# Kernel tuning notes

Measured on AMD Instinct MI355X. Metric: run time of the kernel, lower is better.

The kernel has to match this reference:

```python
import jax, jax.numpy as jnp
import numpy as np

NG, NPG, NF = 256, 64, 64          # graphs, nodes/graph, features (NPG == NF: x is per-graph [N,N])
HC, NL = 504, 4                     # hidden_channels, num_layers (HC*NL == TRIU)
E_PER = 1024                        # edges per graph
ALPHA = 0.5
EPS = 1e-5
TRIU = NF * (NF - 1) // 2           # 2016 strict-upper-triangle entries
HIDDEN, NCLS = 1024, 2


def _bn(x, g, b):
    # BatchNorm1d in training mode: biased batch statistics
    m = x.mean(0)
    v = x.var(0)
    return (x - m) * jax.lax.rsqrt(v + EPS) * g + b


def _gcn(x, src, dst, W, b):
    n = x.shape[0]
    xw = x @ W
    deg = jax.ops.segment_sum(jnp.ones(src.shape[0], x.dtype), dst, num_segments=n) + 1.0
    dinv = jax.lax.rsqrt(deg)
    coef = (dinv[src] * dinv[dst])[:, None]
    agg = jax.ops.segment_sum(xw[src] * coef, dst, num_segments=n)
    return agg + xw * (dinv * dinv)[:, None] + b


def _pool(x, batch):
    # global_mean_pool; every graph has exactly NPG nodes
    return jax.ops.segment_sum(x, batch, num_segments=NG) / NPG


def setup_inputs():
    key = jax.random.key(0)
    ks = jax.random.split(key, 16)
    total = NG * NPG
    x = jax.random.normal(ks[0], (total, NF), jnp.float32)
    offs = (jnp.arange(NG) * NPG)[:, None]
    edge_src = (jax.random.randint(ks[1], (NG, E_PER), 0, NPG) + offs).reshape(-1)
    edge_dst = (jax.random.randint(ks[2], (NG, E_PER), 0, NPG) + offs).reshape(-1)
    batch = jnp.arange(total) // NPG

    def lin(k, fi, fo):
        return jax.random.normal(k, (fi, fo), jnp.float32) / np.sqrt(fi)

    Wg0 = lin(ks[3], NF, HC)
    bg0 = jnp.zeros((HC,), jnp.float32)
    Wg_rest = jax.random.normal(ks[4], (NL - 1, HC, HC), jnp.float32) / np.sqrt(HC)
    bg_rest = jnp.zeros((NL - 1, HC), jnp.float32)
    gx = jnp.ones((TRIU,), jnp.float32); bx = jnp.zeros((TRIU,), jnp.float32)
    gh = jnp.ones((HC * NL,), jnp.float32); bh = jnp.zeros((HC * NL,), jnp.float32)
    Watt = lin(ks[5], TRIU, 1); batt = jnp.zeros((1,), jnp.float32)
    D1 = TRIU + HC * NL  # 4032
    Wm1 = lin(ks[6], D1, HIDDEN); bm1 = jnp.zeros((HIDDEN,), jnp.float32)
    gm1 = jnp.ones((HIDDEN,), jnp.float32); bem1 = jnp.zeros((HIDDEN,), jnp.float32)
    Wm2 = lin(ks[7], HIDDEN, HIDDEN // 2); bm2 = jnp.zeros((HIDDEN // 2,), jnp.float32)
    gm2 = jnp.ones((HIDDEN // 2,), jnp.float32); bem2 = jnp.zeros((HIDDEN // 2,), jnp.float32)
    Wm3 = lin(ks[8], HIDDEN // 2, HIDDEN // 2); bm3 = jnp.zeros((HIDDEN // 2,), jnp.float32)
    gm3 = jnp.ones((HIDDEN // 2,), jnp.float32); bem3 = jnp.zeros((HIDDEN // 2,), jnp.float32)
    Wm4 = lin(ks[9], HIDDEN // 2, NCLS); bm4 = jnp.zeros((NCLS,), jnp.float32)
    return dict(x=x, Wg0=Wg0, bg0=bg0, Wg_rest=Wg_rest, bg_rest=bg_rest, gx=gx, bx=bx,
                gh=gh, bh=bh, Watt=Watt, batt=batt, Wm1=Wm1, bm1=bm1, gm1=gm1, bem1=bem1,
                Wm2=Wm2, bm2=bm2, gm2=gm2, bem2=bem2, Wm3=Wm3, bm3=bm3, gm3=gm3, bem3=bem3,
                Wm4=Wm4, bm4=bm4, edge_src=edge_src, edge_dst=edge_dst, batch=batch)


def reference(x, Wg0, bg0, Wg_rest, bg_rest, gx, bx, gh, bh, Watt, batt,
              Wm1, bm1, gm1, bem1, Wm2, bm2, gm2, bem2, Wm3, bm3, gm3, bem3,
              Wm4, bm4, edge_src, edge_dst, batch):
    # stacked GCN convs (no nonlinearity between convs, as in source)
    cur = _gcn(x, edge_src, edge_dst, Wg0, bg0)
    hs = [_pool(cur, batch)]
    for i in range(NL - 1):
        cur = _gcn(cur, edge_src, edge_dst, Wg_rest[i], bg_rest[i])
        hs.append(_pool(cur, batch))
    h = _bn(jnp.concatenate(hs, axis=1), gh, bh)          # [NG, HC*NL]
    # per-graph strict upper triangle of the [N,N] input matrix (== triu().nonzero() trick)
    iu, ju = jnp.triu_indices(NF, k=1)
    xv = x.reshape(NG, NPG, NF)[:, iu, ju]                # [NG, TRIU]
    xv = _bn(xv, gx, bx)
    att = jax.nn.sigmoid(xv @ Watt + batt)                # [NG, 1]
    xf = att * xv + (1.0 - att) * h * ALPHA               # attention-weighted fusion
    z = jnp.concatenate([xf, h], axis=1)                  # [NG, TRIU + HC*NL]
    z = jax.nn.relu(_bn(z @ Wm1 + bm1, gm1, bem1))
    z = jax.nn.relu(_bn(z @ Wm2 + bm2, gm2, bem2))
    z = jax.nn.relu(_bn(z @ Wm3 + bm3, gm3, bem3))
    return z @ Wm4 + bm4                                   # [NG, NCLS]
```

## Files before the change

### kernel.cpp

```cpp
#include <hip/hip_runtime.h>
#include <math.h>

#define NGRAPH 256
#define NPG 64
#define NFEAT 64
#define HC 504
#define NLAY 4
#define EPER 1024
#define NTRIU 2016
#define DCAT 4032
#define HID1 1024
#define HID2 512

#define GCN_LDS (65536 + 73728 + 18432)
#define AHL_LO 4608

typedef __attribute__((ext_vector_type(8))) short bfrag8;
typedef __attribute__((ext_vector_type(4))) float f32x4;

struct __align__(8) us4 { unsigned short a, b, c, d; };

__device__ __forceinline__ unsigned short f2b(float f) {
    union { float f; unsigned u; } v; v.f = f;
    unsigned r = (v.u + 0x7fffu + ((v.u >> 16) & 1u)) >> 16;
    return (unsigned short)r;
}
__device__ __forceinline__ float b2f(unsigned short h) {
    union { unsigned u; float f; } v; v.u = ((unsigned)h) << 16;
    return v.f;
}

__global__ void conv_gcn(const float* __restrict__ Wg0, const float* __restrict__ WgR,
                         unsigned short* __restrict__ Wt0, unsigned short* __restrict__ Wt123)
{
    const int z = blockIdx.z;
    const float* W;
    unsigned short* W4;
    int K, KL;
    if (z == 0) {
        if (blockIdx.y >= 2) return;
        W = Wg0; W4 = Wt0; K = 64; KL = 64;
    } else {
        W = WgR + (size_t)(z - 1) * HC * HC;
        W4 = Wt123 + (size_t)(z - 1) * 262144;
        K = HC; KL = 512;
    }
    __shared__ float T[32][33];
    int k0 = blockIdx.y * 32, n0 = blockIdx.x * 32;
    int tx = threadIdx.x, ty = threadIdx.y;
#pragma unroll
    for (int j = 0; j < 32; j += 8) {
        int k = k0 + ty + j, n = n0 + tx;
        T[ty + j][tx] = (k < K && n < HC) ? W[(size_t)k * HC + n] : 0.f;
    }
    __syncthreads();
#pragma unroll
    for (int j = 0; j < 32; j += 8) {
        int n = n0 + ty + j, k = k0 + tx;
        int idx = ((n >> 4) * (KL >> 5) + (k >> 5)) * 512
                + (((k >> 3) & 3) << 7) + ((n & 15) << 3) + (k & 7);
        W4[idx] = f2b(T[tx][ty + j]);
    }
}

__global__ void conv_mlp(const float* __restrict__ Wm1, const float* __restrict__ Wm2,
                         const float* __restrict__ Wm3,
                         unsigned short* __restrict__ W1t, unsigned short* __restrict__ W2t,
                         unsigned short* __restrict__ W3t)
{
    const int z = blockIdx.z;
    const float* W;
    unsigned short* Wt;
    int K, N;
    if (z == 0)      { W = Wm1; Wt = W1t; K = DCAT; N = HID1; }
    else if (z == 1) { W = Wm2; Wt = W2t; K = HID1; N = HID2; }
    else             { W = Wm3; Wt = W3t; K = HID2; N = HID2; }
    int k0 = blockIdx.y * 32, n0 = blockIdx.x * 32;
    if (k0 >= K || n0 >= N) return;
    __shared__ float T[32][33];
    int tx = threadIdx.x, ty = threadIdx.y;
#pragma unroll
    for (int j = 0; j < 32; j += 8) {
        int k = k0 + ty + j, n = n0 + tx;
        T[ty + j][tx] = (k < K && n < N) ? W[(size_t)k * N + n] : 0.f;
    }
    __syncthreads();
#pragma unroll
    for (int j = 0; j < 32; j += 8) {
        int n = n0 + ty + j, k = k0 + tx;
        Wt[(size_t)n * K + k] = f2b(T[tx][ty + j]);
    }
}

template<int KL>
__device__ __forceinline__ void gcn_layer(const unsigned short* __restrict__ W4,
                                          const float* __restrict__ bias,
                                          unsigned short* cur, unsigned short* xwt,
                                          const unsigned short* ahl,
                                          float* __restrict__ hsg,
                                          int wv, int lm, int lh)
{
    constexpr int KTS = KL >> 5;
    const int colw = wv << 5;
    const int kswz = (lm & 7) << 3;
    const int lane8 = ((lh << 4) + lm) << 3;

    f32x4 acc[4][2];
#pragma unroll
    for (int m0 = 0; m0 < 4; ++m0)
#pragma unroll
        for (int cc = 0; cc < 2; ++cc) acc[m0][cc] = (f32x4){0.f, 0.f, 0.f, 0.f};

    bfrag8 bq[2][2];
#pragma unroll
    for (int cc = 0; cc < 2; ++cc)
        bq[0][cc] = *(const bfrag8*)(const void*)&W4[(size_t)((wv * 2 + cc) * KTS + 0) * 512 + lane8];
    if (KTS > 1) {
#pragma unroll
        for (int cc = 0; cc < 2; ++cc)
            bq[1][cc] = *(const bfrag8*)(const void*)&W4[(size_t)((wv * 2 + cc) * KTS + 1) * 512 + lane8];
    }
#pragma unroll
    for (int kt = 0; kt < KTS; ++kt) {
        bfrag8 a[4];
#pragma unroll
        for (int m0 = 0; m0 < 4; ++m0)
            a[m0] = *(const bfrag8*)(const void*)&cur[(m0 * 16 + lm) * 512 + ((kt * 32 + (lh << 3)) ^ kswz)];
        bfrag8 bc[2];
        bc[0] = bq[kt & 1][0]; bc[1] = bq[kt & 1][1];
        if (kt + 2 < KTS) {
#pragma unroll
            for (int cc = 0; cc < 2; ++cc)
                bq[kt & 1][cc] = *(const bfrag8*)(const void*)&W4[(size_t)((wv * 2 + cc) * KTS + kt + 2) * 512 + lane8];
        }
#pragma unroll
        for (int cc = 0; cc < 2; ++cc)
#pragma unroll
            for (int m0 = 0; m0 < 4; ++m0)
                acc[m0][cc] = __builtin_amdgcn_mfma_f32_16x16x32_bf16(a[m0], bc[cc], acc[m0][cc], 0, 0, 0);
    }
    __syncthreads();

#pragma unroll
    for (int cc = 0; cc < 2; ++cc) {
        const int c = colw + cc * 16 + lm;
#pragma unroll
        for (int m0 = 0; m0 < 4; ++m0) {
            us4 p;
            p.a = f2b(acc[m0][cc][0]); p.b = f2b(acc[m0][cc][1]);
            p.c = f2b(acc[m0][cc][2]); p.d = f2b(acc[m0][cc][3]);
            *(us4*)(void*)&xwt[c * 72 + m0 * 16 + (lh << 2)] = p;
        }
    }

    f32x4 acc2[2][4];
#pragma unroll
    for (int cc = 0; cc < 2; ++cc)
#pragma unroll
        for (int n0 = 0; n0 < 4; ++n0) acc2[cc][n0] = (f32x4){0.f, 0.f, 0.f, 0.f};
#pragma unroll
    for (int n0 = 0; n0 < 4; ++n0) {
        const int o = (n0 * 16 + lm) * 72 + (lh << 3);
        bfrag8 bh0 = *(const bfrag8*)(const void*)&ahl[o];
        bfrag8 bh1 = *(const bfrag8*)(const void*)&ahl[o + 32];
        bfrag8 bl0 = *(const bfrag8*)(const void*)&ahl[AHL_LO + o];
        bfrag8 bl1 = *(const bfrag8*)(const void*)&ahl[AHL_LO + o + 32];
#pragma unroll
        for (int cc = 0; cc < 2; ++cc) {
            const int c = colw + cc * 16 + lm;
            bfrag8 a0 = *(const bfrag8*)(const void*)&xwt[c * 72 + (lh << 3)];
            bfrag8 a1 = *(const bfrag8*)(const void*)&xwt[c * 72 + 32 + (lh << 3)];
            acc2[cc][n0] = __builtin_amdgcn_mfma_f32_16x16x32_bf16(a0, bh0, acc2[cc][n0], 0, 0, 0);
            acc2[cc][n0] = __builtin_amdgcn_mfma_f32_16x16x32_bf16(a0, bl0, acc2[cc][n0], 0, 0, 0);
            acc2[cc][n0] = __builtin_amdgcn_mfma_f32_16x16x32_bf16(a1, bh1, acc2[cc][n0], 0, 0, 0);
            acc2[cc][n0] = __builtin_amdgcn_mfma_f32_16x16x32_bf16(a1, bl1, acc2[cc][n0], 0, 0, 0);
        }
    }

#pragma unroll
    for (int cc = 0; cc < 2; ++cc) {
        const int cb = colw + cc * 16 + (lh << 2);
        float bv[4];
#pragma unroll
        for (int r = 0; r < 4; ++r) {
            int c = cb + r;
            bv[r] = (c < HC) ? bias[c] : 0.f;
        }
        float t0 = 0.f, t1 = 0.f, t2 = 0.f, t3 = 0.f;
#pragma unroll
        for (int n0 = 0; n0 < 4; ++n0) {
            const int d = n0 * 16 + lm;
            float v0 = acc2[cc][n0][0] + bv[0];
            float v1 = acc2[cc][n0][1] + bv[1];
            float v2 = acc2[cc][n0][2] + bv[2];
            float v3 = acc2[cc][n0][3] + bv[3];
            t0 += v0; t1 += v1; t2 += v2; t3 += v3;
            us4 p;
            p.a = f2b(v0); p.b = f2b(v1); p.c = f2b(v2); p.d = f2b(v3);
            *(us4*)(void*)&cur[d * 512 + (cb ^ ((d & 7) << 3))] = p;
        }
#pragma unroll
        for (int m = 1; m < 16; m <<= 1) {
            t0 += __shfl_xor(t0, m, 64);
            t1 += __shfl_xor(t1, m, 64);
            t2 += __shfl_xor(t2, m, 64);
            t3 += __shfl_xor(t3, m, 64);
        }
        if (lm == 0 && cb < HC)
            *(float4*)&hsg[cb] = make_float4(t0 * (1.0f / 64.0f), t1 * (1.0f / 64.0f),
                                             t2 * (1.0f / 64.0f), t3 * (1.0f / 64.0f));
    }
    __syncthreads();
}

__global__ __launch_bounds__(1024, 4) void gcn_all(const float* __restrict__ x,
                                                   const int* __restrict__ esrc,
                                                   const int* __restrict__ edst,
                                                   const unsigned short* __restrict__ Wt0,
                                                   const unsigned short* __restrict__ Wt123,
                                                   const float* __restrict__ bg0,
                                                   const float* __restrict__ bgR,
                                                   float* __restrict__ hs)
{
    extern __shared__ char lds[];
    unsigned short* cur = (unsigned short*)lds;
    unsigned short* xwt = (unsigned short*)(lds + 65536);
    unsigned short* ahl = (unsigned short*)(lds + 65536 + 73728);
    float* Af   = (float*)(lds + 65536);
    int*   cnt  = (int*)(lds + 65536 + 16384);
    float* dinv = (float*)(lds + 65536 + 16384 + 256);

    const int g = blockIdx.x, tid = threadIdx.x;
    const int wv = tid >> 6, lane = tid & 63;
    const int lm = lane & 15, lh = lane >> 4;

    for (int i = tid; i < 4096; i += 1024) Af[i] = 0.f;
    if (tid < 64) cnt[tid] = 0;
    __syncthreads();
    atomicAdd(&cnt[edst[(size_t)g * EPER + tid] & 63], 1);
    __syncthreads();
    if (tid < 64) dinv[tid] = rsqrtf((float)cnt[tid] + 1.0f);
    __syncthreads();
    {
        int s = esrc[(size_t)g * EPER + tid] & 63;
        int d = edst[(size_t)g * EPER + tid] & 63;
        atomicAdd(&Af[d * 64 + s], dinv[s] * dinv[d]);
    }
    __syncthreads();
    if (tid < 64) Af[tid * 64 + tid] += dinv[tid] * dinv[tid];
    __syncthreads();
    for (int i = tid; i < 4096; i += 1024) {
        float v = Af[i];
        unsigned short h = f2b(v);
        int d = i >> 6, s = i & 63;
        ahl[d * 72 + s] = h;
        ahl[AHL_LO + d * 72 + s] = f2b(v - b2f(h));
    }
    {
        float4 v = ((const float4*)(x + (size_t)g * 4096))[tid];
        int row = (tid * 4) >> 6, col = (tid * 4) & 63;
        unsigned short* p = &cur[row * 512 + (col ^ ((row & 7) << 3))];
        p[0] = f2b(v.x); p[1] = f2b(v.y); p[2] = f2b(v.z); p[3] = f2b(v.w);
    }
    __syncthreads();

    float* hsg = hs + (size_t)g * (HC * NLAY);
    gcn_layer<64>(Wt0, bg0, cur, xwt, ahl, hsg, wv, lm, lh);
    for (int l = 1; l < NLAY; ++l)
        gcn_layer<512>(Wt123 + (size_t)(l - 1) * 262144, bgR + (l - 1) * HC,
                       cur, xwt, ahl, hsg + l * HC, wv, lm, lh);
}

__global__ __launch_bounds__(256) void pre_stats(const float* __restrict__ hs,
                                                 const float* __restrict__ x,
                                                 float* __restrict__ xv,
                                                 float* __restrict__ psh,
                                                 float* __restrict__ pssh,
                                                 float* __restrict__ psx,
                                                 float* __restrict__ pssx)
{
    int t = blockIdx.x * 256 + threadIdx.x;
    if (t >= NTRIU) return;
    int g0 = blockIdx.y * 16;
    if (blockIdx.z == 0) {
        float s = 0.f, ss = 0.f;
        for (int g = g0; g < g0 + 16; ++g) {
            float v = hs[(size_t)g * NTRIU + t];
            s += v; ss += v * v;
        }
        psh [(size_t)blockIdx.y * NTRIU + t] = s;
        pssh[(size_t)blockIdx.y * NTRIU + t] = ss;
    } else {
        int i = (int)(63.5f - sqrtf(63.5f * 63.5f - 2.0f * (float)t));
        while (63 * (i + 1) - (i + 1) * i / 2 <= t) ++i;
        while (63 * i - i * (i - 1) / 2 > t) --i;
        int j = t - (63 * i - i * (i - 1) / 2) + i + 1;
        int o = i * 64 + j;
        float s = 0.f, ss = 0.f;
        for (int g = g0; g < g0 + 16; ++g) {
            float v = x[(size_t)g * 4096 + o];
            xv[(size_t)g * NTRIU + t] = v;
            s += v; ss += v * v;
        }
        psx [(size_t)blockIdx.y * NTRIU + t] = s;
        pssx[(size_t)blockIdx.y * NTRIU + t] = ss;
    }
}

__global__ __launch_bounds__(256) void stats_fin2(const float* __restrict__ psh,
                                                  const float* __restrict__ pssh,
                                                  const float* __restrict__ psx,
                                                  const float* __restrict__ pssx,
                                                  float* __restrict__ hm,
                                                  float* __restrict__ hiv,
                                                  float* __restrict__ xm,
                                                  float* __restrict__ xi)
{
    int f = blockIdx.x * 256 + threadIdx.x;
    if (f >= NTRIU) return;
    const float* ps  = blockIdx.y ? psx  : psh;
    const float* pss = blockIdx.y ? pssx : pssh;
    float* mo = blockIdx.y ? xm : hm;
    float* io = blockIdx.y ? xi : hiv;
    float s = 0.f, ss = 0.f;
    for (int b = 0; b < 16; ++b) {
        s  += ps [(size_t)b * NTRIU + f];
        ss += pss[(size_t)b * NTRIU + f];
    }
    float m = s * (1.0f / NGRAPH);
    mo[f] = m;
    io[f] = rsqrtf(ss * (1.0f / NGRAPH) - m * m + 1e-5f);
}

__global__ __launch_bounds__(256) void attz_fused(const float* __restrict__ xv,
                                                  const float* __restrict__ xm,
                                                  const float* __restrict__ xi,
                                                  const float* __restrict__ gx,
                                                  const float* __restrict__ bx,
                                                  const float* __restrict__ hsrc,
                                                  const float* __restrict__ hm,
                                                  const float* __restrict__ hi,
                                                  const float* __restrict__ gh,
                                                  const float* __restrict__ bh,
                                                  const float* __restrict__ Watt,
                                                  const float* __restrict__ batt,
                                                  unsigned short* __restrict__ zhi,
                                                  unsigned short* __restrict__ zlo)
{
    int g = blockIdx.x;
    __shared__ float xs[NTRIU];
    __shared__ float red[256];
    float s = 0.f;
    for (int t = threadIdx.x; t < NTRIU; t += 256) {
        float v = (xv[(size_t)g * NTRIU + t] - xm[t]) * xi[t] * gx[t] + bx[t];
        xs[t] = v;
        s += v * Watt[t];
    }
    red[threadIdx.x] = s;
    __syncthreads();
    for (int w = 128; w > 0; w >>= 1) {
        if (threadIdx.x < w) red[threadIdx.x] += red[threadIdx.x + w];
        __syncthreads();
    }
    float att = 1.0f / (1.0f + expf(-(red[0] + batt[0])));
    for (int t = threadIdx.x; t < NTRIU; t += 256) {
        float hn = (hsrc[(size_t)g * NTRIU + t] - hm[t]) * hi[t] * gh[t] + bh[t];
        float zf = att * xs[t] + (1.0f - att) * hn * 0.5f;
        unsigned short h0 = f2b(zf);
        zhi[(size_t)g * DCAT + t] = h0;
        zlo[(size_t)g * DCAT + t] = f2b(zf - b2f(h0));
        unsigned short h1 = f2b(hn);
        zhi[(size_t)g * DCAT + NTRIU + t] = h1;
        zlo[(size_t)g * DCAT + NTRIU + t] = f2b(hn - b2f(h1));
    }
}

__global__ __launch_bounds__(256) void gemm_bf_sk(const unsigned short* __restrict__ Ahi,
                                                  const unsigned short* __restrict__ Alo,
                                                  const unsigned short* __restrict__ Bt,
                                                  float* __restrict__ P,
                                                  int N, int K, int chunk)
{
    __shared__ unsigned short Ah[2][2048], Al[2][2048], Bs[2][2048];
    const int tid  = threadIdx.x;
    const int wave = tid >> 6, lane = tid & 63;
    const int row0 = blockIdx.y << 6, col0 = blockIdx.x << 6;
    const int kb = blockIdx.z * chunk;
    const int NT = chunk >> 5;
    const int sr = tid >> 2, sk = (tid & 3) << 3;
    const unsigned short* gAh = Ahi + (size_t)(row0 + sr) * K + kb + sk;
    const unsigned short* gAl = Alo + (size_t)(row0 + sr) * K + kb + sk;
    const unsigned short* gB  = Bt  + (size_t)(col0 + sr) * K + kb + sk;

    int4 rh = *(const int4*)(const void*)gAh;
    int4 rl = *(const int4*)(const void*)gAl;
    int4 rb = *(const int4*)(const void*)gB;
    *(int4*)(void*)&Ah[0][tid << 3] = rh;
    *(int4*)(void*)&Al[0][tid << 3] = rl;
    *(int4*)(void*)&Bs[0][tid << 3] = rb;
    __syncthreads();

    f32x4 acc0 = {0.f, 0.f, 0.f, 0.f};
    f32x4 acc1 = acc0, acc2 = acc0, acc3 = acc0;
    const int aoff = (wave * 16 + (lane & 15)) * 32 + ((lane >> 4) << 3);
    const int boff = (lane & 15) * 32 + ((lane >> 4) << 3);

    for (int t = 0; t < NT; ++t) {
        if (t + 1 < NT) {
            rh = *(const int4*)(const void*)(gAh + (t + 1) * 32);
            rl = *(const int4*)(const void*)(gAl + (t + 1) * 32);
            rb = *(const int4*)(const void*)(gB  + (t + 1) * 32);
        }
        const unsigned short* ah = Ah[t & 1];
        const unsigned short* al = Al[t & 1];
        const unsigned short* bs = Bs[t & 1];
        bfrag8 a  = *(const bfrag8*)(const void*)&ah[aoff];
        bfrag8 a2 = *(const bfrag8*)(const void*)&al[aoff];
        bfrag8 b0 = *(const bfrag8*)(const void*)&bs[boff];
        bfrag8 b1 = *(const bfrag8*)(const void*)&bs[boff + 16 * 32];
        bfrag8 b2 = *(const bfrag8*)(const void*)&bs[boff + 32 * 32];
        bfrag8 b3 = *(const bfrag8*)(const void*)&bs[boff + 48 * 32];
        acc0 = __builtin_amdgcn_mfma_f32_16x16x32_bf16(a,  b0, acc0, 0, 0, 0);
        acc0 = __builtin_amdgcn_mfma_f32_16x16x32_bf16(a2, b0, acc0, 0, 0, 0);
        acc1 = __builtin_amdgcn_mfma_f32_16x16x32_bf16(a,  b1, acc1, 0, 0, 0);
        acc1 = __builtin_amdgcn_mfma_f32_16x16x32_bf16(a2, b1, acc1, 0, 0, 0);
        acc2 = __builtin_amdgcn_mfma_f32_16x16x32_bf16(a,  b2, acc2, 0, 0, 0);
        acc2 = __builtin_amdgcn_mfma_f32_16x16x32_bf16(a2, b2, acc2, 0, 0, 0);
        acc3 = __builtin_amdgcn_mfma_f32_16x16x32_bf16(a,  b3, acc3, 0, 0, 0);
        acc3 = __builtin_amdgcn_mfma_f32_16x16x32_bf16(a2, b3, acc3, 0, 0, 0);
        if (t + 1 < NT) {
            *(int4*)(void*)&Ah[(t + 1) & 1][tid << 3] = rh;
            *(int4*)(void*)&Al[(t + 1) & 1][tid << 3] = rl;
            *(int4*)(void*)&Bs[(t + 1) & 1][tid << 3] = rb;
        }
        __syncthreads();
    }

    float* Pp = P + (size_t)blockIdx.z * NGRAPH * N;
    const int rbase = row0 + wave * 16 + ((lane >> 4) << 2);
    const int cbase = col0 + (lane & 15);
#pragma unroll
    for (int r = 0; r < 4; ++r) {
        int grow = rbase + r;
        Pp[(size_t)grow * N + cbase +  0] = acc0[r];
        Pp[(size_t)grow * N + cbase + 16] = acc1[r];
        Pp[(size_t)grow * N + cbase + 32] = acc2[r];
        Pp[(size_t)grow * N + cbase + 48] = acc3[r];
    }
}

__global__ __launch_bounds__(256) void reduce_stats(const float* __restrict__ P,
                                                    const float* __restrict__ bias,
                                                    float* __restrict__ mf,
                                                    float* __restrict__ ps,
                                                    float* __restrict__ pss,
                                                    int N, int S)
{
    int f = blockIdx.x * 256 + threadIdx.x;
    int r0 = blockIdx.y * 8;
    size_t MN = (size_t)NGRAPH * N;
    float bv = bias[f];
    float s = 0.f, ss = 0.f;
    for (int r = r0; r < r0 + 8; ++r) {
        float v = 0.f;
        for (int t = 0; t < S; ++t) v += P[(size_t)t * MN + (size_t)r * N + f];
        v += bv;
        mf[(size_t)r * N + f] = v;
        s += v; ss += v * v;
    }
    ps [(size_t)blockIdx.y * N + f] = s;
    pss[(size_t)blockIdx.y * N + f] = ss;
}

__global__ __launch_bounds__(256) void fin_apply(const float* __restrict__ ps,
                                                 const float* __restrict__ pss,
                                                 const float* __restrict__ mf,
                                                 const float* __restrict__ gamma,
                                                 const float* __restrict__ beta,
                                                 unsigned short* __restrict__ hi,
                                                 unsigned short* __restrict__ lo,
                                                 int N)
{
    int f = blockIdx.x * 256 + threadIdx.x;
    float s = 0.f, ss = 0.f;
#pragma unroll 8
    for (int b = 0; b < 32; ++b) {
        s  += ps [(size_t)b * N + f];
        ss += pss[(size_t)b * N + f];
    }
    float m  = s * (1.0f / NGRAPH);
    float iv = rsqrtf(ss * (1.0f / NGRAPH) - m * m + 1e-5f) * gamma[f];
    float bt = beta[f];
    int r0 = blockIdx.y * 8;
    for (int r = r0; r < r0 + 8; ++r) {
        float v = (mf[(size_t)r * N + f] - m) * iv + bt;
        v = fmaxf(v, 0.f);
        unsigned short h = f2b(v);
        hi[(size_t)r * N + f] = h;
        lo[(size_t)r * N + f] = f2b(v - b2f(h));
    }
}

__global__ __launch_bounds__(256) void final_kernel(const unsigned short* __restrict__ Xhi,
                                                    const unsigned short* __restrict__ Xlo,
                                                    const float* __restrict__ W,
                                                    const float* __restrict__ b,
                                                    float* __restrict__ out)
{
    int g = blockIdx.x;
    float s0 = 0.f, s1 = 0.f;
    for (int k = threadIdx.x; k < HID2; k += 256) {
        float v = b2f(Xhi[(size_t)g * HID2 + k]) + b2f(Xlo[(size_t)g * HID2 + k]);
        s0 += v * W[k * 2 + 0];
        s1 += v * W[k * 2 + 1];
    }
    __shared__ float r0[256], r1[256];
    r0[threadIdx.x] = s0; r1[threadIdx.x] = s1;
    __syncthreads();
    for (int w = 128; w > 0; w >>= 1) {
        if (threadIdx.x < w) {
            r0[threadIdx.x] += r0[threadIdx.x + w];
            r1[threadIdx.x] += r1[threadIdx.x + w];
        }
        __syncthreads();
    }
    if (threadIdx.x == 0) {
        out[g * 2 + 0] = r0[0] + b[0];
        out[g * 2 + 1] = r1[0] + b[1];
    }
}

extern "C" void kernel_launch(void* const* d_in, const int* in_sizes, int n_in,
                              void* d_out, int out_size, void* d_ws, size_t ws_size,
                              hipStream_t stream)
{
    const float* x      = (const float*)d_in[0];
    const float* Wg0    = (const float*)d_in[1];
    const float* bg0    = (const float*)d_in[2];
    const float* WgR    = (const float*)d_in[3];
    const float* bgR    = (const float*)d_in[4];
    const float* gx     = (const float*)d_in[5];
    const float* bx     = (const float*)d_in[6];
    const float* gh     = (const float*)d_in[7];
    const float* bh     = (const float*)d_in[8];
    const float* Watt   = (const float*)d_in[9];
    const float* batt   = (const float*)d_in[10];
    const float* Wm1    = (const float*)d_in[11];
    const float* bm1    = (const float*)d_in[12];
    const float* gm1    = (const float*)d_in[13];
    const float* bem1   = (const float*)d_in[14];
    const float* Wm2    = (const float*)d_in[15];
    const float* bm2    = (const float*)d_in[16];
    const float* gm2    = (const float*)d_in[17];
    const float* bem2   = (const float*)d_in[18];
    const float* Wm3    = (const float*)d_in[19];
    const float* bm3    = (const float*)d_in[20];
    const float* gm3    = (const float*)d_in[21];
    const float* bem3   = (const float*)d_in[22];
    const float* Wm4    = (const float*)d_in[23];
    const float* bm4    = (const float*)d_in[24];
    const int*   esrc   = (const int*)d_in[25];
    const int*   edst   = (const int*)d_in[26];
    float* out = (float*)d_out;

    char* w = (char*)d_ws;
    auto alloc = [&](size_t bytes) -> char* {
        char* p = w;
        w += (bytes + 255) & ~(size_t)255;
        return p;
    };
    unsigned short* Wt0   = (unsigned short*)alloc((size_t)512 * 64 * 2);
    unsigned short* Wt123 = (unsigned short*)alloc((size_t)3 * 512 * 512 * 2);
    unsigned short* W1t   = (unsigned short*)alloc((size_t)HID1 * DCAT * 2);
    unsigned short* W2t   = (unsigned short*)alloc((size_t)HID2 * HID1 * 2);
    unsigned short* W3t   = (unsigned short*)alloc((size_t)HID2 * HID2 * 2);
    float*          hs    = (float*)alloc((size_t)NGRAPH * NTRIU * 4);
    float*          xv    = (float*)alloc((size_t)NGRAPH * NTRIU * 4);
    unsigned short* zhi   = (unsigned short*)alloc((size_t)NGRAPH * DCAT * 2);
    unsigned short* zlo   = (unsigned short*)alloc((size_t)NGRAPH * DCAT * 2);
    float*          P     = (float*)alloc((size_t)8 * NGRAPH * HID1 * 4);
    float*          mf    = (float*)alloc((size_t)NGRAPH * HID1 * 4);
    unsigned short* m1hi  = (unsigned short*)alloc((size_t)NGRAPH * HID1 * 2);
    unsigned short* m1lo  = (unsigned short*)alloc((size_t)NGRAPH * HID1 * 2);
    unsigned short* m2hi  = (unsigned short*)alloc((size_t)NGRAPH * HID2 * 2);
    unsigned short* m2lo  = (unsigned short*)alloc((size_t)NGRAPH * HID2 * 2);
    unsigned short* m3hi  = (unsigned short*)alloc((size_t)NGRAPH * HID2 * 2);
    unsigned short* m3lo  = (unsigned short*)alloc((size_t)NGRAPH * HID2 * 2);
    float*          psh   = (float*)alloc((size_t)16 * NTRIU * 4);
    float*          pssh  = (float*)alloc((size_t)16 * NTRIU * 4);
    float*          psx   = (float*)alloc((size_t)16 * NTRIU * 4);
    float*          pssx  = (float*)alloc((size_t)16 * NTRIU * 4);
    float*          ps    = (float*)alloc((size_t)32 * HID1 * 4);
    float*          pss   = (float*)alloc((size_t)32 * HID1 * 4);
    float*          xm    = (float*)alloc(NTRIU * 4);
    float*          xi    = (float*)alloc(NTRIU * 4);
    float*          hm    = (float*)alloc(NTRIU * 4);
    float*          hiv   = (float*)alloc(NTRIU * 4);

    hipFuncSetAttribute((const void*)gcn_all,
                        hipFuncAttributeMaxDynamicSharedMemorySize, GCN_LDS);

    conv_gcn<<<dim3(16, 16, 4), dim3(32, 8), 0, stream>>>(Wg0, WgR, Wt0, Wt123);
    conv_mlp<<<dim3(32, 126, 3), dim3(32, 8), 0, stream>>>(Wm1, Wm2, Wm3, W1t, W2t, W3t);

    gcn_all<<<NGRAPH, 1024, GCN_LDS, stream>>>(x, esrc, edst, Wt0, Wt123, bg0, bgR, hs);

    pre_stats<<<dim3(8, 16, 2), 256, 0, stream>>>(hs, x, xv, psh, pssh, psx, pssx);
    stats_fin2<<<dim3(8, 2), 256, 0, stream>>>(psh, pssh, psx, pssx, hm, hiv, xm, xi);
    attz_fused<<<NGRAPH, 256, 0, stream>>>(xv, xm, xi, gx, bx, hs, hm, hiv, gh, bh,
                                           Watt, batt, zhi, zlo);

    gemm_bf_sk<<<dim3(16, 4, 7), 256, 0, stream>>>(zhi, zlo, W1t, P, HID1, DCAT, 576);
    reduce_stats<<<dim3(4, 32), 256, 0, stream>>>(P, bm1, mf, ps, pss, HID1, 7);
    fin_apply<<<dim3(4, 32), 256, 0, stream>>>(ps, pss, mf, gm1, bem1, m1hi, m1lo, HID1);

    gemm_bf_sk<<<dim3(8, 4, 8), 256, 0, stream>>>(m1hi, m1lo, W2t, P, HID2, HID1, 128);
    reduce_stats<<<dim3(2, 32), 256, 0, stream>>>(P, bm2, mf, ps, pss, HID2, 8);
    fin_apply<<<dim3(2, 32), 256, 0, stream>>>(ps, pss, mf, gm2, bem2, m2hi, m2lo, HID2);

    gemm_bf_sk<<<dim3(8, 4, 8), 256, 0, stream>>>(m2hi, m2lo, W3t, P, HID2, HID2, 64);
    reduce_stats<<<dim3(2, 32), 256, 0, stream>>>(P, bm3, mf, ps, pss, HID2, 8);
    fin_apply<<<dim3(2, 32), 256, 0, stream>>>(ps, pss, mf, gm3, bem3, m3hi, m3lo, HID2);

    final_kernel<<<NGRAPH, 256, 0, stream>>>(m3hi, m3lo, Wm4, bm4, out);
}
```

Before: 162.2 us.

## Fuse post-GCN tail kernels into one cooperative kernel with grid syncs

Replaces the thirteen separate launches after the GCN stage (stats, attention fusion, three split-K GEMMs with their BN reduce/apply passes, and the final linear layer) with a single cooperative kernel of 256 blocks. The phases are separated by grid.sync() calls. The aim is to remove per-launch overhead and inter-kernel gaps in this latency-bound tail. In exchange, every phase is capped at 256 blocks, so the first GEMM's 448 jobs take two passes per block. Idle blocks in small phases still pay the cost of each grid barrier.

```diff
diff --git a/kernel.cpp b/kernel.cpp
--- a/kernel.cpp
+++ b/kernel.cpp
@@ -1,5 +1,8 @@
 #include <hip/hip_runtime.h>
+#include <hip/hip_cooperative_groups.h>
 #include <math.h>
+
+namespace cg = cooperative_groups;
 
 #define NGRAPH 256
 #define NPG 64
@@ -271,121 +274,17 @@
                        cur, xwt, ahl, hsg + l * HC, wv, lm, lh);
 }
 
-__global__ __launch_bounds__(256) void pre_stats(const float* __restrict__ hs,
-                                                 const float* __restrict__ x,
-                                                 float* __restrict__ xv,
-                                                 float* __restrict__ psh,
-                                                 float* __restrict__ pssh,
-                                                 float* __restrict__ psx,
-                                                 float* __restrict__ pssx)
-{
-    int t = blockIdx.x * 256 + threadIdx.x;
-    if (t >= NTRIU) return;
-    int g0 = blockIdx.y * 16;
-    if (blockIdx.z == 0) {
-        float s = 0.f, ss = 0.f;
-        for (int g = g0; g < g0 + 16; ++g) {
-            float v = hs[(size_t)g * NTRIU + t];
-            s += v; ss += v * v;
-        }
-        psh [(size_t)blockIdx.y * NTRIU + t] = s;
-        pssh[(size_t)blockIdx.y * NTRIU + t] = ss;
-    } else {
-        int i = (int)(63.5f - sqrtf(63.5f * 63.5f - 2.0f * (float)t));
-        while (63 * (i + 1) - (i + 1) * i / 2 <= t) ++i;
-        while (63 * i - i * (i - 1) / 2 > t) --i;
-        int j = t - (63 * i - i * (i - 1) / 2) + i + 1;
-        int o = i * 64 + j;
-        float s = 0.f, ss = 0.f;
-        for (int g = g0; g < g0 + 16; ++g) {
-            float v = x[(size_t)g * 4096 + o];
-            xv[(size_t)g * NTRIU + t] = v;
-            s += v; ss += v * v;
-        }
-        psx [(size_t)blockIdx.y * NTRIU + t] = s;
-        pssx[(size_t)blockIdx.y * NTRIU + t] = ss;
-    }
-}
-
-__global__ __launch_bounds__(256) void stats_fin2(const float* __restrict__ psh,
-                                                  const float* __restrict__ pssh,
-                                                  const float* __restrict__ psx,
-                                                  const float* __restrict__ pssx,
-                                                  float* __restrict__ hm,
-                                                  float* __restrict__ hiv,
-                                                  float* __restrict__ xm,
-                                                  float* __restrict__ xi)
-{
-    int f = blockIdx.x * 256 + threadIdx.x;
-    if (f >= NTRIU) return;
-    const float* ps  = blockIdx.y ? psx  : psh;
-    const float* pss = blockIdx.y ? pssx : pssh;
-    float* mo = blockIdx.y ? xm : hm;
-    float* io = blockIdx.y ? xi : hiv;
-    float s = 0.f, ss = 0.f;
-    for (int b = 0; b < 16; ++b) {
-        s  += ps [(size_t)b * NTRIU + f];
-        ss += pss[(size_t)b * NTRIU + f];
-    }
-    float m = s * (1.0f / NGRAPH);
-    mo[f] = m;
-    io[f] = rsqrtf(ss * (1.0f / NGRAPH) - m * m + 1e-5f);
-}
-
-__global__ __launch_bounds__(256) void attz_fused(const float* __restrict__ xv,
-                                                  const float* __restrict__ xm,
-                                                  const float* __restrict__ xi,
-                                                  const float* __restrict__ gx,
-                                                  const float* __restrict__ bx,
-                                                  const float* __restrict__ hsrc,
-                                                  const float* __restrict__ hm,
-                                                  const float* __restrict__ hi,
-                                                  const float* __restrict__ gh,
-                                                  const float* __restrict__ bh,
-                                                  const float* __restrict__ Watt,
-                                                  const float* __restrict__ batt,
-                                                  unsigned short* __restrict__ zhi,
-                                                  unsigned short* __restrict__ zlo)
-{
-    int g = blockIdx.x;
-    __shared__ float xs[NTRIU];
-    __shared__ float red[256];
-    float s = 0.f;
-    for (int t = threadIdx.x; t < NTRIU; t += 256) {
-        float v = (xv[(size_t)g * NTRIU + t] - xm[t]) * xi[t] * gx[t] + bx[t];
-        xs[t] = v;
-        s += v * Watt[t];
-    }
-    red[threadIdx.x] = s;
-    __syncthreads();
-    for (int w = 128; w > 0; w >>= 1) {
-        if (threadIdx.x < w) red[threadIdx.x] += red[threadIdx.x + w];
-        __syncthreads();
-    }
-    float att = 1.0f / (1.0f + expf(-(red[0] + batt[0])));
-    for (int t = threadIdx.x; t < NTRIU; t += 256) {
-        float hn = (hsrc[(size_t)g * NTRIU + t] - hm[t]) * hi[t] * gh[t] + bh[t];
-        float zf = att * xs[t] + (1.0f - att) * hn * 0.5f;
-        unsigned short h0 = f2b(zf);
-        zhi[(size_t)g * DCAT + t] = h0;
-        zlo[(size_t)g * DCAT + t] = f2b(zf - b2f(h0));
-        unsigned short h1 = f2b(hn);
-        zhi[(size_t)g * DCAT + NTRIU + t] = h1;
-        zlo[(size_t)g * DCAT + NTRIU + t] = f2b(hn - b2f(h1));
-    }
-}
-
-__global__ __launch_bounds__(256) void gemm_bf_sk(const unsigned short* __restrict__ Ahi,
-                                                  const unsigned short* __restrict__ Alo,
-                                                  const unsigned short* __restrict__ Bt,
-                                                  float* __restrict__ P,
-                                                  int N, int K, int chunk)
-{
-    __shared__ unsigned short Ah[2][2048], Al[2][2048], Bs[2][2048];
-    const int tid  = threadIdx.x;
+__device__ __forceinline__ void gemm_job(const unsigned short* __restrict__ Ahi,
+                                         const unsigned short* __restrict__ Alo,
+                                         const unsigned short* __restrict__ Bt,
+                                         float* __restrict__ P,
+                                         int N, int K, int chunk, int bx, int by, int bz,
+                                         unsigned short* sAh, unsigned short* sAl,
+                                         unsigned short* sBs, int tid)
+{
     const int wave = tid >> 6, lane = tid & 63;
-    const int row0 = blockIdx.y << 6, col0 = blockIdx.x << 6;
-    const int kb = blockIdx.z * chunk;
+    const int row0 = by << 6, col0 = bx << 6;
+    const int kb = bz * chunk;
     const int NT = chunk >> 5;
     const int sr = tid >> 2, sk = (tid & 3) << 3;
     const unsigned short* gAh = Ahi + (size_t)(row0 + sr) * K + kb + sk;
@@ -395,9 +294,9 @@
     int4 rh = *(const int4*)(const void*)gAh;
     int4 rl = *(const int4*)(const void*)gAl;
     int4 rb = *(const int4*)(const void*)gB;
-    *(int4*)(void*)&Ah[0][tid << 3] = rh;
-    *(int4*)(void*)&Al[0][tid << 3] = rl;
-    *(int4*)(void*)&Bs[0][tid << 3] = rb;
+    *(int4*)(void*)&sAh[tid << 3] = rh;
+    *(int4*)(void*)&sAl[tid << 3] = rl;
+    *(int4*)(void*)&sBs[tid << 3] = rb;
     __syncthreads();
 
     f32x4 acc0 = {0.f, 0.f, 0.f, 0.f};
@@ -411,15 +310,13 @@
             rl = *(const int4*)(const void*)(gAl + (t + 1) * 32);
             rb = *(const int4*)(const void*)(gB  + (t + 1) * 32);
         }
-        const unsigned short* ah = Ah[t & 1];
-        const unsigned short* al = Al[t & 1];
-        const unsigned short* bs = Bs[t & 1];
-        bfrag8 a  = *(const bfrag8*)(const void*)&ah[aoff];
-        bfrag8 a2 = *(const bfrag8*)(const void*)&al[aoff];
-        bfrag8 b0 = *(const bfrag8*)(const void*)&bs[boff];
-        bfrag8 b1 = *(const bfrag8*)(const void*)&bs[boff + 16 * 32];
-        bfrag8 b2 = *(const bfrag8*)(const void*)&bs[boff + 32 * 32];
-        bfrag8 b3 = *(const bfrag8*)(const void*)&bs[boff + 48 * 32];
+        const int bo = (t & 1) * 2048;
+        bfrag8 a  = *(const bfrag8*)(const void*)&sAh[bo + aoff];
+        bfrag8 a2 = *(const bfrag8*)(const void*)&sAl[bo + aoff];
+        bfrag8 b0 = *(const bfrag8*)(const void*)&sBs[bo + boff];
+        bfrag8 b1 = *(const bfrag8*)(const void*)&sBs[bo + boff + 16 * 32];
+        bfrag8 b2 = *(const bfrag8*)(const void*)&sBs[bo + boff + 32 * 32];
+        bfrag8 b3 = *(const bfrag8*)(const void*)&sBs[bo + boff + 48 * 32];
         acc0 = __builtin_amdgcn_mfma_f32_16x16x32_bf16(a,  b0, acc0, 0, 0, 0);
         acc0 = __builtin_amdgcn_mfma_f32_16x16x32_bf16(a2, b0, acc0, 0, 0, 0);
         acc1 = __builtin_amdgcn_mfma_f32_16x16x32_bf16(a,  b1, acc1, 0, 0, 0);
@@ -429,14 +326,15 @@
         acc3 = __builtin_amdgcn_mfma_f32_16x16x32_bf16(a,  b3, acc3, 0, 0, 0);
         acc3 = __builtin_amdgcn_mfma_f32_16x16x32_bf16(a2, b3, acc3, 0, 0, 0);
         if (t + 1 < NT) {
-            *(int4*)(void*)&Ah[(t + 1) & 1][tid << 3] = rh;
-            *(int4*)(void*)&Al[(t + 1) & 1][tid << 3] = rl;
-            *(int4*)(void*)&Bs[(t + 1) & 1][tid << 3] = rb;
+            const int bn = ((t + 1) & 1) * 2048;
+            *(int4*)(void*)&sAh[bn + (tid << 3)] = rh;
+            *(int4*)(void*)&sAl[bn + (tid << 3)] = rl;
+            *(int4*)(void*)&sBs[bn + (tid << 3)] = rb;
         }
         __syncthreads();
     }
 
-    float* Pp = P + (size_t)blockIdx.z * NGRAPH * N;
+    float* Pp = P + (size_t)bz * NGRAPH * N;
     const int rbase = row0 + wave * 16 + ((lane >> 4) << 2);
     const int cbase = col0 + (lane & 15);
 #pragma unroll
@@ -449,15 +347,13 @@
     }
 }
 
-__global__ __launch_bounds__(256) void reduce_stats(const float* __restrict__ P,
-                                                    const float* __restrict__ bias,
-                                                    float* __restrict__ mf,
-                                                    float* __restrict__ ps,
-                                                    float* __restrict__ pss,
-                                                    int N, int S)
-{
-    int f = blockIdx.x * 256 + threadIdx.x;
-    int r0 = blockIdx.y * 8;
+__device__ __forceinline__ void rs_job(const float* __restrict__ P, const float* __restrict__ bias,
+                                       float* __restrict__ mf, float* __restrict__ ps,
+                                       float* __restrict__ pss, int N, int S,
+                                       int xj, int yj, int tid)
+{
+    int f = xj * 256 + tid;
+    int r0 = yj * 8;
     size_t MN = (size_t)NGRAPH * N;
     float bv = bias[f];
     float s = 0.f, ss = 0.f;
@@ -468,20 +364,17 @@
         mf[(size_t)r * N + f] = v;
         s += v; ss += v * v;
     }
-    ps [(size_t)blockIdx.y * N + f] = s;
-    pss[(size_t)blockIdx.y * N + f] = ss;
-}
-
-__global__ __launch_bounds__(256) void fin_apply(const float* __restrict__ ps,
-                                                 const float* __restrict__ pss,
-                                                 const float* __restrict__ mf,
-                                                 const float* __restrict__ gamma,
-                                                 const float* __restrict__ beta,
-                                                 unsigned short* __restrict__ hi,
-                                                 unsigned short* __restrict__ lo,
-                                                 int N)
-{
-    int f = blockIdx.x * 256 + threadIdx.x;
+    ps [(size_t)yj * N + f] = s;
+    pss[(size_t)yj * N + f] = ss;
+}
+
+__device__ __forceinline__ void fa_job(const float* __restrict__ ps, const float* __restrict__ pss,
+                                       const float* __restrict__ mf,
+                                       const float* __restrict__ gamma, const float* __restrict__ beta,
+                                       unsigned short* __restrict__ hi, unsigned short* __restrict__ lo,
+                                       int N, int xj, int yj, int tid)
+{
+    int f = xj * 256 + tid;
     float s = 0.f, ss = 0.f;
 #pragma unroll 8
     for (int b = 0; b < 32; ++b) {
@@ -491,7 +384,7 @@
     float m  = s * (1.0f / NGRAPH);
     float iv = rsqrtf(ss * (1.0f / NGRAPH) - m * m + 1e-5f) * gamma[f];
     float bt = beta[f];
-    int r0 = blockIdx.y * 8;
+    int r0 = yj * 8;
     for (int r = r0; r < r0 + 8; ++r) {
         float v = (mf[(size_t)r * N + f] - m) * iv + bt;
         v = fmaxf(v, 0.f);
@@ -501,32 +394,162 @@
     }
 }
 
-__global__ __launch_bounds__(256) void final_kernel(const unsigned short* __restrict__ Xhi,
-                                                    const unsigned short* __restrict__ Xlo,
-                                                    const float* __restrict__ W,
-                                                    const float* __restrict__ b,
-                                                    float* __restrict__ out)
-{
-    int g = blockIdx.x;
-    float s0 = 0.f, s1 = 0.f;
-    for (int k = threadIdx.x; k < HID2; k += 256) {
-        float v = b2f(Xhi[(size_t)g * HID2 + k]) + b2f(Xlo[(size_t)g * HID2 + k]);
-        s0 += v * W[k * 2 + 0];
-        s1 += v * W[k * 2 + 1];
-    }
-    __shared__ float r0[256], r1[256];
-    r0[threadIdx.x] = s0; r1[threadIdx.x] = s1;
-    __syncthreads();
-    for (int w = 128; w > 0; w >>= 1) {
-        if (threadIdx.x < w) {
-            r0[threadIdx.x] += r0[threadIdx.x + w];
-            r1[threadIdx.x] += r1[threadIdx.x + w];
-        }
+struct TailArgs {
+    const float* x; const float* hs; float* xv;
+    float* psh; float* pssh; float* psx; float* pssx;
+    float* hm; float* hiv; float* xm; float* xi;
+    const float* gx; const float* bx; const float* gh; const float* bh;
+    const float* Watt; const float* batt;
+    unsigned short* zhi; unsigned short* zlo;
+    const unsigned short* W1t; const unsigned short* W2t; const unsigned short* W3t;
+    const float* bm1; const float* gm1; const float* bem1;
+    const float* bm2; const float* gm2; const float* bem2;
+    const float* bm3; const float* gm3; const float* bem3;
+    const float* Wm4; const float* bm4;
+    float* P; float* mf;
+    unsigned short* m1hi; unsigned short* m1lo;
+    unsigned short* m2hi; unsigned short* m2lo;
+    unsigned short* m3hi; unsigned short* m3lo;
+    float* ps; float* pss;
+    float* out;
+};
+
+__global__ __launch_bounds__(256, 1) void tail_coop(TailArgs a)
+{
+    cg::grid_group grid = cg::this_grid();
+    __shared__ __align__(16) char smem[24576];
+    unsigned short* sAh = (unsigned short*)smem;
+    unsigned short* sAl = sAh + 4096;
+    unsigned short* sBs = sAl + 4096;
+    float* xs   = (float*)smem;
+    float* redv = (float*)(smem + 8064);
+    const int bid = blockIdx.x, tid = threadIdx.x;
+
+    {
+        int xj = bid & 7, yj = (bid >> 3) & 15, zj = bid >> 7;
+        int t = xj * 256 + tid;
+        if (t < NTRIU) {
+            int g0 = yj * 16;
+            if (zj == 0) {
+                float s = 0.f, ss = 0.f;
+                for (int g = g0; g < g0 + 16; ++g) {
+                    float v = a.hs[(size_t)g * NTRIU + t];
+                    s += v; ss += v * v;
+                }
+                a.psh [(size_t)yj * NTRIU + t] = s;
+                a.pssh[(size_t)yj * NTRIU + t] = ss;
+            } else {
+                int i = (int)(63.5f - sqrtf(63.5f * 63.5f - 2.0f * (float)t));
+                while (63 * (i + 1) - (i + 1) * i / 2 <= t) ++i;
+                while (63 * i - i * (i - 1) / 2 > t) --i;
+                int j = t - (63 * i - i * (i - 1) / 2) + i + 1;
+                int o = i * 64 + j;
+                float s = 0.f, ss = 0.f;
+                for (int g = g0; g < g0 + 16; ++g) {
+                    float v = a.x[(size_t)g * 4096 + o];
+                    a.xv[(size_t)g * NTRIU + t] = v;
+                    s += v; ss += v * v;
+                }
+                a.psx [(size_t)yj * NTRIU + t] = s;
+                a.pssx[(size_t)yj * NTRIU + t] = ss;
+            }
+        }
+    }
+    grid.sync();
+    if (bid < 16) {
+        int xj = bid & 7, yj = bid >> 3;
+        int f = xj * 256 + tid;
+        if (f < NTRIU) {
+            const float* ps  = yj ? a.psx  : a.psh;
+            const float* pss = yj ? a.pssx : a.pssh;
+            float* mo = yj ? a.xm : a.hm;
+            float* io = yj ? a.xi : a.hiv;
+            float s = 0.f, ss = 0.f;
+            for (int b = 0; b < 16; ++b) {
+                s  += ps [(size_t)b * NTRIU + f];
+                ss += pss[(size_t)b * NTRIU + f];
+            }
+            float m = s * (1.0f / NGRAPH);
+            mo[f] = m;
+            io[f] = rsqrtf(ss * (1.0f / NGRAPH) - m * m + 1e-5f);
+        }
+    }
+    grid.sync();
+    {
+        int g = bid;
+        float s = 0.f;
+        for (int t = tid; t < NTRIU; t += 256) {
+            float v = (a.xv[(size_t)g * NTRIU + t] - a.xm[t]) * a.xi[t] * a.gx[t] + a.bx[t];
+            xs[t] = v;
+            s += v * a.Watt[t];
+        }
+        redv[tid] = s;
         __syncthreads();
-    }
-    if (threadIdx.x == 0) {
-        out[g * 2 + 0] = r0[0] + b[0];
-        out[g * 2 + 1] = r1[0] + b[1];
+        for (int w2 = 128; w2 > 0; w2 >>= 1) {
+            if (tid < w2) redv[tid] += redv[tid + w2];
+            __syncthreads();
+        }
+        float att = 1.0f / (1.0f + expf(-(redv[0] + a.batt[0])));
+        __syncthreads();
+        for (int t = tid; t < NTRIU; t += 256) {
+            float hn = (a.hs[(size_t)g * NTRIU + t] - a.hm[t]) * a.hiv[t] * a.gh[t] + a.bh[t];
+            float zf = att * xs[t] + (1.0f - att) * hn * 0.5f;
+            unsigned short h0 = f2b(zf);
+            a.zhi[(size_t)g * DCAT + t] = h0;
+            a.zlo[(size_t)g * DCAT + t] = f2b(zf - b2f(h0));
+            unsigned short h1 = f2b(hn);
+            a.zhi[(size_t)g * DCAT + NTRIU + t] = h1;
+            a.zlo[(size_t)g * DCAT + NTRIU + t] = f2b(hn - b2f(h1));
+        }
+    }
+    grid.sync();
+    for (int job = bid; job < 448; job += 256) {
+        gemm_job(a.zhi, a.zlo, a.W1t, a.P, HID1, DCAT, 576,
+                 job & 15, (job >> 4) & 3, job >> 6, sAh, sAl, sBs, tid);
+        __syncthreads();
+    }
+    grid.sync();
+    if (bid < 128) rs_job(a.P, a.bm1, a.mf, a.ps, a.pss, HID1, 7, bid & 3, bid >> 2, tid);
+    grid.sync();
+    if (bid < 128) fa_job(a.ps, a.pss, a.mf, a.gm1, a.bem1, a.m1hi, a.m1lo,
+                          HID1, bid & 3, bid >> 2, tid);
+    grid.sync();
+    gemm_job(a.m1hi, a.m1lo, a.W2t, a.P, HID2, HID1, 128,
+             bid & 7, (bid >> 3) & 3, bid >> 5, sAh, sAl, sBs, tid);
+    grid.sync();
+    if (bid < 64) rs_job(a.P, a.bm2, a.mf, a.ps, a.pss, HID2, 8, bid & 1, bid >> 1, tid);
+    grid.sync();
+    if (bid < 64) fa_job(a.ps, a.pss, a.mf, a.gm2, a.bem2, a.m2hi, a.m2lo,
+                         HID2, bid & 1, bid >> 1, tid);
+    grid.sync();
+    gemm_job(a.m2hi, a.m2lo, a.W3t, a.P, HID2, HID2, 64,
+             bid & 7, (bid >> 3) & 3, bid >> 5, sAh, sAl, sBs, tid);
+    grid.sync();
+    if (bid < 64) rs_job(a.P, a.bm3, a.mf, a.ps, a.pss, HID2, 8, bid & 1, bid >> 1, tid);
+    grid.sync();
+    if (bid < 64) fa_job(a.ps, a.pss, a.mf, a.gm3, a.bem3, a.m3hi, a.m3lo,
+                         HID2, bid & 1, bid >> 1, tid);
+    grid.sync();
+    {
+        int g = bid;
+        float s0 = 0.f, s1 = 0.f;
+        for (int k = tid; k < HID2; k += 256) {
+            float v = b2f(a.m3hi[(size_t)g * HID2 + k]) + b2f(a.m3lo[(size_t)g * HID2 + k]);
+            s0 += v * a.Wm4[k * 2 + 0];
+            s1 += v * a.Wm4[k * 2 + 1];
+        }
+        float* r0 = (float*)smem;
+        float* r1 = r0 + 256;
+        r0[tid] = s0; r1[tid] = s1;
+        __syncthreads();
+        for (int w2 = 128; w2 > 0; w2 >>= 1) {
+            if (tid < w2) { r0[tid] += r0[tid + w2]; r1[tid] += r1[tid + w2]; }
+            __syncthreads();
+        }
+        if (tid == 0) {
+            a.out[g * 2 + 0] = r0[0] + a.bm4[0];
+            a.out[g * 2 + 1] = r1[0] + a.bm4[1];
+        }
     }
 }
 
@@ -605,22 +628,25 @@
 
     gcn_all<<<NGRAPH, 1024, GCN_LDS, stream>>>(x, esrc, edst, Wt0, Wt123, bg0, bgR, hs);
 
-    pre_stats<<<dim3(8, 16, 2), 256, 0, stream>>>(hs, x, xv, psh, pssh, psx, pssx);
-    stats_fin2<<<dim3(8, 2), 256, 0, stream>>>(psh, pssh, psx, pssx, hm, hiv, xm, xi);
-    attz_fused<<<NGRAPH, 256, 0, stream>>>(xv, xm, xi, gx, bx, hs, hm, hiv, gh, bh,
-                                           Watt, batt, zhi, zlo);
-
-    gemm_bf_sk<<<dim3(16, 4, 7), 256, 0, stream>>>(zhi, zlo, W1t, P, HID1, DCAT, 576);
-    reduce_stats<<<dim3(4, 32), 256, 0, stream>>>(P, bm1, mf, ps, pss, HID1, 7);
-    fin_apply<<<dim3(4, 32), 256, 0, stream>>>(ps, pss, mf, gm1, bem1, m1hi, m1lo, HID1);
-
-    gemm_bf_sk<<<dim3(8, 4, 8), 256, 0, stream>>>(m1hi, m1lo, W2t, P, HID2, HID1, 128);
-    reduce_stats<<<dim3(2, 32), 256, 0, stream>>>(P, bm2, mf, ps, pss, HID2, 8);
-    fin_apply<<<dim3(2, 32), 256, 0, stream>>>(ps, pss, mf, gm2, bem2, m2hi, m2lo, HID2);
-
-    gemm_bf_sk<<<dim3(8, 4, 8), 256, 0, stream>>>(m2hi, m2lo, W3t, P, HID2, HID2, 64);
-    reduce_stats<<<dim3(2, 32), 256, 0, stream>>>(P, bm3, mf, ps, pss, HID2, 8);
-    fin_apply<<<dim3(2, 32), 256, 0, stream>>>(ps, pss, mf, gm3, bem3, m3hi, m3lo, HID2);
-
-    final_kernel<<<NGRAPH, 256, 0, stream>>>(m3hi, m3lo, Wm4, bm4, out);
-}
+    TailArgs ta;
+    ta.x = x; ta.hs = hs; ta.xv = xv;
+    ta.psh = psh; ta.pssh = pssh; ta.psx = psx; ta.pssx = pssx;
+    ta.hm = hm; ta.hiv = hiv; ta.xm = xm; ta.xi = xi;
+    ta.gx = gx; ta.bx = bx; ta.gh = gh; ta.bh = bh;
+    ta.Watt = Watt; ta.batt = batt;
+    ta.zhi = zhi; ta.zlo = zlo;
+    ta.W1t = W1t; ta.W2t = W2t; ta.W3t = W3t;
+    ta.bm1 = bm1; ta.gm1 = gm1; ta.bem1 = bem1;
+    ta.bm2 = bm2; ta.gm2 = gm2; ta.bem2 = bem2;
+    ta.bm3 = bm3; ta.gm3 = gm3; ta.bem3 = bem3;
+    ta.Wm4 = Wm4; ta.bm4 = bm4;
+    ta.P = P; ta.mf = mf;
+    ta.m1hi = m1hi; ta.m1lo = m1lo;
+    ta.m2hi = m2hi; ta.m2lo = m2lo;
+    ta.m3hi = m3hi; ta.m3lo = m3lo;
+    ta.ps = ps; ta.pss = pss;
+    ta.out = out;
+    void* kargs[] = { &ta };
+    hipLaunchCooperativeKernel((const void*)tail_coop, dim3(256), dim3(256),
+                               kargs, 0, stream);
+}
```

Result: slower. 476.9 us (+194.1%).
